# Kernel tuning notes

Hardware: AMD Instinct MI355X
Metric: run time of the kernel (lower is better)

Reference implementation:

```python
import jax, jax.numpy as jnp
import numpy as np

B, L, D_MODEL, H = 2, 2048, 2048, 16
HD = D_MODEL // H  # 128 head dim
EPS = 1e-6


def rms_norm(x, scale):
    # float32 RMSNorm over last dim, per Flux QKNorm
    x32 = x.astype(jnp.float32)
    rrms = jax.lax.rsqrt(jnp.mean(x32 * x32, axis=-1, keepdims=True) + EPS)
    return (x32 * rrms) * scale


def apply_rope(xq, xk, freqs_cis):
    # xq, xk: [B, L, H, D]; freqs_cis: [1, L, 1, D/2, 2, 2]
    shp = xq.shape
    xq_ = xq.astype(jnp.float32).reshape(*shp[:-1], -1, 1, 2)
    xk_ = xk.astype(jnp.float32).reshape(*shp[:-1], -1, 1, 2)
    xq_out = freqs_cis[..., 0] * xq_[..., 0] + freqs_cis[..., 1] * xq_[..., 1]
    xk_out = freqs_cis[..., 0] * xk_[..., 0] + freqs_cis[..., 1] * xk_[..., 1]
    return xq_out.reshape(shp).astype(xq.dtype), xk_out.reshape(shp).astype(xk.dtype)


def setup_inputs() -> dict:
    key = jax.random.key(0)
    k1, k2, k3, k4 = jax.random.split(key, 4)
    x = jax.random.normal(k1, (B, L, D_MODEL), dtype=jnp.float32)
    pe = jax.random.normal(k2, (1, L, 1, HD // 2, 2, 2), dtype=jnp.float32)
    w_qkv = jax.random.normal(k3, (D_MODEL, 3 * D_MODEL), dtype=jnp.float32) * (D_MODEL ** -0.5)
    w_proj = jax.random.normal(k4, (D_MODEL, D_MODEL), dtype=jnp.float32) * (D_MODEL ** -0.5)
    q_scale = jnp.ones((HD,), dtype=jnp.float32)
    k_scale = jnp.ones((HD,), dtype=jnp.float32)
    return {"x": x, "pe": pe, "w_qkv": w_qkv, "w_proj": w_proj,
            "q_scale": q_scale, "k_scale": k_scale}


def reference(x, pe, w_qkv, w_proj, q_scale, k_scale):
    qkv = x @ w_qkv                                  # [B, L, 3*H*D]
    qkv = qkv.reshape(B, L, 3, H, HD)
    q, k, v = qkv[:, :, 0], qkv[:, :, 1], qkv[:, :, 2]  # [B, L, H, D]
    # QK RMSNorm (cast back to v's dtype, per QKNorm.forward)
    q = rms_norm(q, q_scale).astype(v.dtype)
    k = rms_norm(k, k_scale).astype(v.dtype)
    # RoPE
    q, k = apply_rope(q, k, pe)
    # non-causal SDPA
    scale = HD ** -0.5
    scores = jnp.einsum('blhd,bmhd->bhlm', q, k) * scale
    attn = jax.nn.softmax(scores, axis=-1)
    out = jnp.einsum('bhlm,bmhd->blhd', attn, v)     # [B, L, H, D]
    out = out.reshape(B, L, H * HD)
    return out @ w_proj
```

## Files before the change

### kernel.cpp

```cpp
#include <hip/hip_runtime.h>

typedef unsigned short u16;
typedef __bf16 bf16x8 __attribute__((ext_vector_type(8)));
typedef float f32x4 __attribute__((ext_vector_type(4)));

#define DEV static __device__ __forceinline__

constexpr int Bc  = 2;
constexpr int Lc  = 2048;
constexpr int Dc  = 2048;
constexpr int Hc  = 16;
constexpr int HDc = 128;
constexpr int Mc  = Bc * Lc;
constexpr int N3c = 3 * Dc;

DEV u16 f2bf(float f) {
  unsigned u = __builtin_bit_cast(unsigned, f);
  u += 0x7fffu + ((u >> 16) & 1u);
  return (u16)(u >> 16);
}
DEV float bf2f(u16 h) { return __builtin_bit_cast(float, ((unsigned)h) << 16); }

DEV void load16(const void* g, void* l) {
  __builtin_amdgcn_global_load_lds(
      (__attribute__((address_space(1))) void*)(g),
      (__attribute__((address_space(3))) void*)(l), 16, 0, 0);
}

__global__ __launch_bounds__(256) void k_prep(const float* __restrict__ x,
                                              const float* __restrict__ w_qkv,
                                              const float* __restrict__ w_proj,
                                              u16* __restrict__ xb,
                                              u16* __restrict__ wqkvT,
                                              u16* __restrict__ wpT) {
  __shared__ u16 t[128 * 136];
  int bid = blockIdx.x;
  int tid = threadIdx.x;
  if (bid < 4096) {
    int i = bid * 256 + tid;
    const float4* s = (const float4*)x;
    float4 a = s[2 * i], b = s[2 * i + 1];
    uint4 o;
    o.x = f2bf(a.x) | ((unsigned)f2bf(a.y) << 16);
    o.y = f2bf(a.z) | ((unsigned)f2bf(a.w) << 16);
    o.z = f2bf(b.x) | ((unsigned)f2bf(b.y) << 16);
    o.w = f2bf(b.z) | ((unsigned)f2bf(b.w) << 16);
    ((uint4*)xb)[i] = o;
    return;
  }
  const float* src;
  u16* dst;
  int tiles_c;
  long ss;
  if (bid < 4096 + 768) {
    int bx = bid - 4096;
    src = w_qkv; dst = wqkvT; tiles_c = 48; ss = N3c;
    int tr = bx / tiles_c, tc = bx % tiles_c;
    src += (long)tr * 128 * ss + tc * 128;
    dst += (long)(tc * 128) * Dc + tr * 128;
  } else {
    int bx = bid - 4864;
    src = w_proj; dst = wpT; tiles_c = 16; ss = Dc;
    int tr = bx / tiles_c, tc = bx % tiles_c;
    src += (long)tr * 128 * ss + tc * 128;
    dst += (long)(tc * 128) * Dc + tr * 128;
  }
#pragma unroll
  for (int p = 0; p < 16; p++) {
    int r = p * 8 + (tid >> 5);
    int c4 = (tid & 31) * 4;
    float4 v = *(const float4*)(src + (long)r * ss + c4);
    t[(c4 + 0) * 136 + r] = f2bf(v.x);
    t[(c4 + 1) * 136 + r] = f2bf(v.y);
    t[(c4 + 2) * 136 + r] = f2bf(v.z);
    t[(c4 + 3) * 136 + r] = f2bf(v.w);
  }
  __syncthreads();
#pragma unroll
  for (int p = 0; p < 8; p++) {
    int c = p * 16 + (tid >> 4);
    int r8 = (tid & 15) * 8;
    uint4 v = *(const uint4*)&t[c * 136 + r8];
    *(uint4*)(dst + (long)c * Dc + r8) = v;
  }
}

__global__ __launch_bounds__(256) void k_vtrans(const u16* __restrict__ qkvb,
                                                u16* __restrict__ Vt) {
  int lt = blockIdx.x;
  int bh = blockIdx.y;
  int b = bh >> 4, h = bh & 15;
  const u16* s = qkvb + (long)(b * Lc + lt * 128) * N3c + 2 * Dc + h * HDc;
  u16* d = Vt + (long)bh * HDc * Lc + lt * 128;
  __shared__ u16 t[128 * 136];
  int tid = threadIdx.x;
#pragma unroll
  for (int p = 0; p < 8; p++) {
    int r = p * 16 + (tid >> 4);
    int c = (tid & 15) * 8;
    uint4 v = *(const uint4*)(s + (long)r * N3c + c);
    const u16* pv = (const u16*)&v;
#pragma unroll
    for (int j = 0; j < 8; j++) t[(c + j) * 136 + r] = pv[j];
  }
  __syncthreads();
#pragma unroll
  for (int p = 0; p < 8; p++) {
    int c = p * 16 + (tid >> 4);
    int r8 = (tid & 15) * 8;
    *(uint4*)(d + (long)c * Lc + r8) = *(const uint4*)&t[c * 136 + r8];
  }
}

DEV void cstore(float* p, float v) { *p = v; }
DEV void cstore(u16* p, float v) { *p = f2bf(v); }

template <typename OT>
__global__ __launch_bounds__(256) void k_gemm(const u16* __restrict__ A,
                                              const u16* __restrict__ Bt,
                                              OT* __restrict__ C, int M, int N,
                                              int K) {
  __shared__ u16 sA[128 * 64], sB[128 * 64];
  int nb = N >> 7;
  int brow = blockIdx.x / nb, bcol = blockIdx.x % nb;
  int tid = threadIdx.x, w = tid >> 6, lane = tid & 63;
  int wr = w >> 1, wc = w & 1, quad = lane >> 4, l15 = lane & 15;
  int lr = lane >> 3, lc = lane & 7;
  const u16* Ab = A + ((long)(brow * 128 + w * 32 + lr)) * K + (lc ^ lr) * 8;
  const u16* Bb = Bt + ((long)(bcol * 128 + w * 32 + lr)) * K + (lc ^ lr) * 8;
  u16* sAw = sA + (w * 32) * 64;
  u16* sBw = sB + (w * 32) * 64;
  f32x4 acc[4][4] = {};
  for (int k0 = 0; k0 < K; k0 += 64) {
    __syncthreads();
#pragma unroll
    for (int i = 0; i < 4; i++) {
      load16(Ab + (long)i * 8 * K + k0, sAw + i * 8 * 64);
      load16(Bb + (long)i * 8 * K + k0, sBw + i * 8 * 64);
    }
    __syncthreads();
#pragma unroll
    for (int kk = 0; kk < 2; kk++) {
      bf16x8 af[4], bfr[4];
#pragma unroll
      for (int mi = 0; mi < 4; mi++) {
        int r = wr * 64 + mi * 16 + l15;
        af[mi] = *(const bf16x8*)&sA[r * 64 + (((kk * 4 + quad) ^ (r & 7)) << 3)];
      }
#pragma unroll
      for (int ni = 0; ni < 4; ni++) {
        int r = wc * 64 + ni * 16 + l15;
        bfr[ni] = *(const bf16x8*)&sB[r * 64 + (((kk * 4 + quad) ^ (r & 7)) << 3)];
      }
#pragma unroll
      for (int mi = 0; mi < 4; mi++)
#pragma unroll
        for (int ni = 0; ni < 4; ni++)
          acc[mi][ni] =
              __builtin_amdgcn_mfma_f32_16x16x32_bf16(af[mi], bfr[ni], acc[mi][ni], 0, 0, 0);
    }
  }
  long orow = (long)brow * 128 + wr * 64;
  int ocol = bcol * 128 + wc * 64;
#pragma unroll
  for (int mi = 0; mi < 4; mi++)
#pragma unroll
    for (int ni = 0; ni < 4; ni++)
#pragma unroll
      for (int r = 0; r < 4; r++)
        cstore(&C[(orow + mi * 16 + quad * 4 + r) * (long)N + ocol + ni * 16 + l15],
               acc[mi][ni][r]);
}

__global__ __launch_bounds__(256) void k_rmsrope(const u16* __restrict__ qkvb,
                                                 const float* __restrict__ pe,
                                                 const float* __restrict__ qsc,
                                                 const float* __restrict__ ksc,
                                                 u16* __restrict__ Qr,
                                                 u16* __restrict__ Kr) {
  int row = blockIdx.x;
  int l = row & (Lc - 1);
  int b = row >> 11;
  int tid = threadIdx.x;
  int h = tid >> 4, s16 = tid & 15;
  int d0 = s16 * 8;
  const u16* qp = qkvb + (long)row * N3c + h * HDc + d0;
  uint4 qv = *(const uint4*)qp;
  uint4 kv = *(const uint4*)(qp + Dc);
  const u16* qu = (const u16*)&qv;
  const u16* ku = (const u16*)&kv;
  float q[8], k[8];
#pragma unroll
  for (int j = 0; j < 8; j++) {
    q[j] = bf2f(qu[j]);
    k[j] = bf2f(ku[j]);
  }
  float sq = 0.f, sk = 0.f;
#pragma unroll
  for (int j = 0; j < 8; j++) {
    sq += q[j] * q[j];
    sk += k[j] * k[j];
  }
#pragma unroll
  for (int m = 1; m < 16; m <<= 1) {
    sq += __shfl_xor(sq, m);
    sk += __shfl_xor(sk, m);
  }
  float rq = rsqrtf(sq * (1.f / HDc) + 1e-6f);
  float rk = rsqrtf(sk * (1.f / HDc) + 1e-6f);
  float qs8[8], ks8[8];
  *(float4*)&qs8[0] = *(const float4*)(qsc + d0);
  *(float4*)&qs8[4] = *(const float4*)(qsc + d0 + 4);
  *(float4*)&ks8[0] = *(const float4*)(ksc + d0);
  *(float4*)&ks8[4] = *(const float4*)(ksc + d0 + 4);
#pragma unroll
  for (int j = 0; j < 8; j++) {
    q[j] *= rq * qs8[j];
    k[j] *= rk * ks8[j];
  }
  float e[16];
  const float* pep = pe + (long)l * 256 + s16 * 16;
#pragma unroll
  for (int j = 0; j < 4; j++) *(float4*)&e[j * 4] = *(const float4*)(pep + j * 4);
  float qo[8], ko[8];
#pragma unroll
  for (int p = 0; p < 4; p++) {
    float e00 = e[p * 4 + 0], e01 = e[p * 4 + 1];
    float e10 = e[p * 4 + 2], e11 = e[p * 4 + 3];
    qo[2 * p]     = e00 * q[2 * p] + e01 * q[2 * p + 1];
    qo[2 * p + 1] = e10 * q[2 * p] + e11 * q[2 * p + 1];
    ko[2 * p]     = e00 * k[2 * p] + e01 * k[2 * p + 1];
    ko[2 * p + 1] = e10 * k[2 * p] + e11 * k[2 * p + 1];
  }
  constexpr float RS = 0.08838834764831845f;
  uint4 oq, ok;
  oq.x = f2bf(qo[0] * RS) | ((unsigned)f2bf(qo[1] * RS) << 16);
  oq.y = f2bf(qo[2] * RS) | ((unsigned)f2bf(qo[3] * RS) << 16);
  oq.z = f2bf(qo[4] * RS) | ((unsigned)f2bf(qo[5] * RS) << 16);
  oq.w = f2bf(qo[6] * RS) | ((unsigned)f2bf(qo[7] * RS) << 16);
  ok.x = f2bf(ko[0]) | ((unsigned)f2bf(ko[1]) << 16);
  ok.y = f2bf(ko[2]) | ((unsigned)f2bf(ko[3]) << 16);
  ok.z = f2bf(ko[4]) | ((unsigned)f2bf(ko[5]) << 16);
  ok.w = f2bf(ko[6]) | ((unsigned)f2bf(ko[7]) << 16);
  long o = (((long)(b * Hc + h)) * Lc + l) * HDc + d0;
  *(uint4*)(Qr + o) = oq;
  *(uint4*)(Kr + o) = ok;
}

__global__ __launch_bounds__(256, 3) void k_attn(const u16* __restrict__ Qr,
                                                 const u16* __restrict__ Kr,
                                                 const u16* __restrict__ Vt,
                                                 u16* __restrict__ Ao) {
  __shared__ u16 smem[24576];
  u16* sQ = smem;
  u16* sK = smem + 8192;
  u16* sV = smem + 16384;
  u16* sP = sQ;
  int bx = blockIdx.x;
  int bh = (bx & 7) | ((bx >> 8) << 3);
  int lt = (bx >> 3) & 31;
  const u16* Qg = Qr + ((long)bh * Lc + lt * 64) * HDc;
  const u16* Kg = Kr + (long)bh * Lc * HDc;
  const u16* Vg = Vt + (long)bh * HDc * Lc;
  int tid = threadIdx.x, w = tid >> 6, lane = tid & 63;
  int quad = lane >> 4, l15 = lane & 15;
  int wsl = w >> 1, wsm = w & 1;
  int wd = w >> 1, wl2 = w & 1;

#pragma unroll
  for (int i = 0; i < 4; i++) {
    int r = i * 16 + w * 4 + quad;
    int gch = l15 ^ (r & 15);
    load16(Qg + (long)r * HDc + gch * 8, sQ + (i * 16 + w * 4) * 128);
  }
  __syncthreads();
  bf16x8 qf[2][4];
#pragma unroll
  for (int mi = 0; mi < 2; mi++) {
    int l = wsl * 32 + mi * 16 + l15;
#pragma unroll
    for (int kk = 0; kk < 4; kk++)
      qf[mi][kk] = *(const bf16x8*)&sQ[l * 128 + (((kk * 4 + quad) ^ l15) << 3)];
  }

  f32x4 o[4][2] = {};
  float rs[8] = {};
  for (int t = 0; t < 32; t++) {
    int m0 = t * 64;
    __syncthreads();
#pragma unroll
    for (int i = 0; i < 4; i++) {
      int r = i * 16 + w * 4 + quad;
      int gch = l15 ^ (r & 15);
      load16(Kg + ((long)(m0 + r)) * HDc + gch * 8, sK + (i * 16 + w * 4) * 128);
    }
#pragma unroll
    for (int i = 0; i < 4; i++) {
      int r = i * 32 + w * 8 + (lane >> 3);
      int gch = (lane & 7) ^ (r & 7);
      load16(Vg + (long)r * Lc + m0 + gch * 8, sV + (i * 32 + w * 8) * 64);
    }
    __syncthreads();
    f32x4 s[2][2] = {};
#pragma unroll
    for (int kk = 0; kk < 4; kk++) {
      bf16x8 bk[2];
#pragma unroll
      for (int ni = 0; ni < 2; ni++) {
        int m = wsm * 32 + ni * 16 + l15;
        bk[ni] = *(const bf16x8*)&sK[m * 128 + (((kk * 4 + quad) ^ l15) << 3)];
      }
#pragma unroll
      for (int mi = 0; mi < 2; mi++)
#pragma unroll
        for (int ni = 0; ni < 2; ni++)
          s[mi][ni] =
              __builtin_amdgcn_mfma_f32_16x16x32_bf16(qf[mi][kk], bk[ni], s[mi][ni], 0, 0, 0);
    }
#pragma unroll
    for (int mi = 0; mi < 2; mi++)
#pragma unroll
      for (int ni = 0; ni < 2; ni++) {
        int pc = wsm * 32 + ni * 16 + l15;
#pragma unroll
        for (int r = 0; r < 4; r++) {
          int pr = wsl * 32 + mi * 16 + quad * 4 + r;
          float p = __expf(s[mi][ni][r]);
          rs[mi * 4 + r] += p;
          unsigned u = __builtin_bit_cast(unsigned, p) + 0x8000u;
          sP[pr * 64 + ((((pc >> 3) ^ (pr & 7)) << 3) | (pc & 7))] = (u16)(u >> 16);
        }
      }
    __syncthreads();
#pragma unroll
    for (int kk = 0; kk < 2; kk++) {
      bf16x8 av[4], bp[2];
#pragma unroll
      for (int mi = 0; mi < 4; mi++) {
        int d = wd * 64 + mi * 16 + l15;
        av[mi] = *(const bf16x8*)&sV[d * 64 + (((kk * 4 + quad) ^ (d & 7)) << 3)];
      }
#pragma unroll
      for (int ni = 0; ni < 2; ni++) {
        int l = wl2 * 32 + ni * 16 + l15;
        bp[ni] = *(const bf16x8*)&sP[l * 64 + (((kk * 4 + quad) ^ (l & 7)) << 3)];
      }
#pragma unroll
      for (int mi = 0; mi < 4; mi++)
#pragma unroll
        for (int ni = 0; ni < 2; ni++)
          o[mi][ni] =
              __builtin_amdgcn_mfma_f32_16x16x32_bf16(av[mi], bp[ni], o[mi][ni], 0, 0, 0);
    }
  }
  __syncthreads();
  float* red  = (float*)sK;
  float* rsum = (float*)sV;
#pragma unroll
  for (int mi = 0; mi < 2; mi++)
#pragma unroll
    for (int r = 0; r < 4; r++) {
      int l = wsl * 32 + mi * 16 + quad * 4 + r;
      red[l * 33 + wsm * 16 + l15] = rs[mi * 4 + r];
    }
  __syncthreads();
  if (tid < 64) {
    float a = 0.f;
#pragma unroll
    for (int j = 0; j < 32; j++) a += red[tid * 33 + j];
    rsum[tid] = a;
  }
  __syncthreads();
  int b = bh >> 4, h = bh & 15;
#pragma unroll
  for (int ni = 0; ni < 2; ni++) {
    int l = wl2 * 32 + ni * 16 + l15;
    float inv = 1.f / rsum[l];
    long rowb = ((long)(b * Lc + lt * 64 + l)) * Dc + h * HDc;
#pragma unroll
    for (int mi = 0; mi < 4; mi++) {
      int d = wd * 64 + mi * 16 + quad * 4;
      ushort4 pk;
      pk.x = f2bf(o[mi][ni][0] * inv);
      pk.y = f2bf(o[mi][ni][1] * inv);
      pk.z = f2bf(o[mi][ni][2] * inv);
      pk.w = f2bf(o[mi][ni][3] * inv);
      *(ushort4*)(Ao + rowb + d) = pk;
    }
  }
}

extern "C" void kernel_launch(void* const* d_in, const int* in_sizes, int n_in,
                              void* d_out, int out_size, void* d_ws, size_t ws_size,
                              hipStream_t stream) {
  const float* x      = (const float*)d_in[0];
  const float* pe     = (const float*)d_in[1];
  const float* w_qkv  = (const float*)d_in[2];
  const float* w_proj = (const float*)d_in[3];
  const float* qs     = (const float*)d_in[4];
  const float* ks     = (const float*)d_in[5];
  float* out = (float*)d_out;
  char* ws = (char*)d_ws;

  u16* xb    = (u16*)(ws);
  u16* wqkvT = (u16*)(ws + 16777216);
  u16* wpT   = (u16*)(ws + 41943040);
  u16* qkvb  = (u16*)(ws + 50331648);
  u16* Qr    = (u16*)(ws + 100663296);
  u16* Kr    = (u16*)(ws + 117440512);
  u16* Vtw   = (u16*)(ws + 134217728);
  u16* Ao    = (u16*)(ws + 150994944);

  k_prep<<<5120, 256, 0, stream>>>(x, w_qkv, w_proj, xb, wqkvT, wpT);
  k_gemm<u16><<<32 * 48, 256, 0, stream>>>(xb, wqkvT, qkvb, Mc, N3c, Dc);
  k_rmsrope<<<Mc, 256, 0, stream>>>(qkvb, pe, qs, ks, Qr, Kr);
  k_vtrans<<<dim3(16, 32), 256, 0, stream>>>(qkvb, Vtw);
  k_attn<<<32 * 32, 256, 0, stream>>>(Qr, Kr, Vtw, Ao);
  k_gemm<float><<<32 * 16, 256, 0, stream>>>(Ao, wpT, out, Mc, Dc, Dc);
}
```

Baseline: 432.3 us.

## Replace GEMM with 256-row 8-wave double-buffered pipelined kernel

Replaces the simple 128x128 single-buffered GEMM with an 8-wave, 512-thread kernel using 256xBN tiles. It double-buffers LDS, interleaves global-to-LDS prefetch with quarter-tile MFMA phases under explicit waitcnt and barriers, and raises MFMA priority with s_setprio. It also remaps block IDs in groups of eight, likely to improve L2 locality across the grid. The intent is to hide load latency and raise data reuse for both the QKV and output projections. In exchange it needs much more LDS and more registers, and the hand-written vmcnt accounting is fragile. The output GEMM also launches only 256 blocks, which may underfill the device.

Measured after the change: 434.1 us. Within noise of the previous version (+0.4%).

```diff
diff --git a/kernel.cpp b/kernel.cpp
--- a/kernel.cpp
+++ b/kernel.cpp
@@ -115,61 +115,156 @@
 DEV void cstore(float* p, float v) { *p = v; }
 DEV void cstore(u16* p, float v) { *p = f2bf(v); }
 
-template <typename OT>
-__global__ __launch_bounds__(256) void k_gemm(const u16* __restrict__ A,
-                                              const u16* __restrict__ Bt,
-                                              OT* __restrict__ C, int M, int N,
-                                              int K) {
-  __shared__ u16 sA[128 * 64], sB[128 * 64];
-  int nb = N >> 7;
-  int brow = blockIdx.x / nb, bcol = blockIdx.x % nb;
+template <int BN, typename OT>
+__global__ __launch_bounds__(512, 2) void k_gemm8(const u16* __restrict__ A,
+                                                  const u16* __restrict__ Bt,
+                                                  OT* __restrict__ C,
+                                                  int M, int N, int K) {
+  constexpr int WN = BN / 4;
+  constexpr int NF = WN / 16;
+  constexpr int BH = BN / 128;
+  __shared__ __align__(16) u16 sA[2][256 * 64];
+  __shared__ __align__(16) u16 sB[2][BN * 64];
+
+  int nb = N / BN;
+  int q8 = gridDim.x >> 3;
+  int sid = (blockIdx.x & 7) * q8 + (blockIdx.x >> 3);
+  int brow = sid / nb, bcol = sid % nb;
+
   int tid = threadIdx.x, w = tid >> 6, lane = tid & 63;
-  int wr = w >> 1, wc = w & 1, quad = lane >> 4, l15 = lane & 15;
+  int wm = w >> 2, wn = w & 3;
+  int quad = lane >> 4, l15 = lane & 15;
   int lr = lane >> 3, lc = lane & 7;
-  const u16* Ab = A + ((long)(brow * 128 + w * 32 + lr)) * K + (lc ^ lr) * 8;
-  const u16* Bb = Bt + ((long)(bcol * 128 + w * 32 + lr)) * K + (lc ^ lr) * 8;
-  u16* sAw = sA + (w * 32) * 64;
-  u16* sBw = sB + (w * 32) * 64;
-  f32x4 acc[4][4] = {};
-  for (int k0 = 0; k0 < K; k0 += 64) {
-    __syncthreads();
-#pragma unroll
-    for (int i = 0; i < 4; i++) {
-      load16(Ab + (long)i * 8 * K + k0, sAw + i * 8 * 64);
-      load16(Bb + (long)i * 8 * K + k0, sBw + i * 8 * 64);
-    }
-    __syncthreads();
-#pragma unroll
-    for (int kk = 0; kk < 2; kk++) {
-      bf16x8 af[4], bfr[4];
-#pragma unroll
-      for (int mi = 0; mi < 4; mi++) {
-        int r = wr * 64 + mi * 16 + l15;
-        af[mi] = *(const bf16x8*)&sA[r * 64 + (((kk * 4 + quad) ^ (r & 7)) << 3)];
-      }
-#pragma unroll
-      for (int ni = 0; ni < 4; ni++) {
-        int r = wc * 64 + ni * 16 + l15;
-        bfr[ni] = *(const bf16x8*)&sB[r * 64 + (((kk * 4 + quad) ^ (r & 7)) << 3)];
-      }
-#pragma unroll
-      for (int mi = 0; mi < 4; mi++)
-#pragma unroll
-        for (int ni = 0; ni < 4; ni++)
-          acc[mi][ni] =
-              __builtin_amdgcn_mfma_f32_16x16x32_bf16(af[mi], bfr[ni], acc[mi][ni], 0, 0, 0);
-    }
-  }
-  long orow = (long)brow * 128 + wr * 64;
-  int ocol = bcol * 128 + wc * 64;
-#pragma unroll
-  for (int mi = 0; mi < 4; mi++)
-#pragma unroll
-    for (int ni = 0; ni < 4; ni++)
+  int NT = K >> 6;
+
+  const u16* Ag = A + (long)(brow * 256 + w * 8 + lr) * K + (lc ^ lr) * 8;
+  const u16* Bg = Bt + (long)(bcol * BN + w * 8 + lr) * K + (lc ^ lr) * 8;
+
+  f32x4 acc[8][NF] = {};
+  bf16x8 a[4][2];
+  bf16x8 b[2][NF / 2][2];
+
+#define STAGE_A8(c, t, h)                                                      \
+  if ((t) < NT) {                                                              \
+    _Pragma("unroll") for (int j = 0; j < 2; j++)                              \
+        load16(Ag + ((long)((h)*128 + j * 64)) * K + (long)(t)*64,             \
+               &sA[c][((h)*128 + j * 64 + w * 8) * 64]);                       \
+  }
+#define STAGE_B8(c, t, h)                                                      \
+  if ((t) < NT) {                                                              \
+    _Pragma("unroll") for (int j = 0; j < BH; j++)                             \
+        load16(Bg + ((long)((h) * (BN / 2) + j * 64)) * K + (long)(t)*64,      \
+               &sB[c][((h) * (BN / 2) + j * 64 + w * 8) * 64]);                \
+  }
+#define LDA8(c, qm)                                                            \
+  _Pragma("unroll") for (int mi = 0; mi < 4; mi++) {                           \
+    int r = wm * 128 + ((qm)*4 + mi) * 16 + l15;                               \
+    _Pragma("unroll") for (int kk = 0; kk < 2; kk++)                           \
+        a[mi][kk] =                                                            \
+        *(const bf16x8*)&sA[c][r * 64 + (((kk * 4 + quad) ^ (r & 7)) << 3)];   \
+  }
+#define LDB8(c, qn)                                                            \
+  _Pragma("unroll") for (int fi = 0; fi < NF / 2; fi++) {                      \
+    int rn = wn * WN + ((qn) * (NF / 2) + fi) * 16 + l15;                      \
+    _Pragma("unroll") for (int kk = 0; kk < 2; kk++)                           \
+        b[qn][fi][kk] =                                                        \
+        *(const bf16x8*)&sB[c][rn * 64 + (((kk * 4 + quad) ^ (rn & 7)) << 3)]; \
+  }
+#define MFMAQ(qm, qn)                                                          \
+  _Pragma("unroll") for (int mi = 0; mi < 4; mi++)                             \
+  _Pragma("unroll") for (int fi = 0; fi < NF / 2; fi++)                        \
+  _Pragma("unroll") for (int kk = 0; kk < 2; kk++)                             \
+      acc[(qm)*4 + mi][(qn) * (NF / 2) + fi] =                                 \
+          __builtin_amdgcn_mfma_f32_16x16x32_bf16(                             \
+              a[mi][kk], b[qn][fi][kk],                                        \
+              acc[(qm)*4 + mi][(qn) * (NF / 2) + fi], 0, 0, 0);
+#define BAR8() __builtin_amdgcn_s_barrier()
+#define LGKM08()                                     \
+  asm volatile("s_waitcnt lgkmcnt(0)" ::: "memory"); \
+  __builtin_amdgcn_sched_barrier(0)
+#define VMC_STEADY8()                                      \
+  do {                                                     \
+    if constexpr (BH == 2)                                 \
+      asm volatile("s_waitcnt vmcnt(4)" ::: "memory");     \
+    else                                                   \
+      asm volatile("s_waitcnt vmcnt(2)" ::: "memory");     \
+  } while (0)
+
+#define TILE8(c, t)                                                            \
+  {                                                                            \
+    LDA8(c, 0);                                                                \
+    LDB8(c, 0);                                                                \
+    STAGE_A8((c) ^ 1, (t) + 1, 0);                                             \
+    BAR8();                                                                    \
+    LGKM08();                                                                  \
+    __builtin_amdgcn_s_setprio(1);                                             \
+    MFMAQ(0, 0);                                                               \
+    __builtin_amdgcn_s_setprio(0);                                             \
+    BAR8();                                                                    \
+    LDB8(c, 1);                                                                \
+    STAGE_A8((c) ^ 1, (t) + 1, 1);                                             \
+    BAR8();                                                                    \
+    LGKM08();                                                                  \
+    __builtin_amdgcn_s_setprio(1);                                             \
+    MFMAQ(0, 1);                                                               \
+    __builtin_amdgcn_s_setprio(0);                                             \
+    BAR8();                                                                    \
+    LDA8(c, 1);                                                                \
+    STAGE_B8(c, (t) + 2, 0);                                                   \
+    BAR8();                                                                    \
+    LGKM08();                                                                  \
+    __builtin_amdgcn_s_setprio(1);                                             \
+    MFMAQ(1, 1);                                                               \
+    __builtin_amdgcn_s_setprio(0);                                             \
+    BAR8();                                                                    \
+    STAGE_B8(c, (t) + 2, 1);                                                   \
+    BAR8();                                                                    \
+    __builtin_amdgcn_s_setprio(1);                                             \
+    MFMAQ(1, 0);                                                               \
+    __builtin_amdgcn_s_setprio(0);                                             \
+    if ((t) < NT - 2) {                                                        \
+      VMC_STEADY8();                                                           \
+    } else {                                                                   \
+      asm volatile("s_waitcnt vmcnt(0)" ::: "memory");                         \
+    }                                                                          \
+    __builtin_amdgcn_sched_barrier(0);                                         \
+    BAR8();                                                                    \
+  }
+
+  STAGE_A8(0, 0, 0);
+  STAGE_A8(0, 0, 1);
+  STAGE_B8(0, 0, 0);
+  STAGE_B8(0, 0, 1);
+  STAGE_B8(1, 1, 0);
+  STAGE_B8(1, 1, 1);
+  VMC_STEADY8();
+  __builtin_amdgcn_sched_barrier(0);
+  BAR8();
+
+  for (int kt = 0; kt < NT; kt += 2) {
+    TILE8(0, kt);
+    TILE8(1, kt + 1);
+  }
+
+  long orow = (long)brow * 256 + wm * 128;
+  int ocol = bcol * BN + wn * WN;
+#pragma unroll
+  for (int mi = 0; mi < 8; mi++)
+#pragma unroll
+    for (int ni = 0; ni < NF; ni++)
 #pragma unroll
       for (int r = 0; r < 4; r++)
         cstore(&C[(orow + mi * 16 + quad * 4 + r) * (long)N + ocol + ni * 16 + l15],
                acc[mi][ni][r]);
+#undef STAGE_A8
+#undef STAGE_B8
+#undef LDA8
+#undef LDB8
+#undef MFMAQ
+#undef BAR8
+#undef LGKM08
+#undef VMC_STEADY8
+#undef TILE8
 }
 
 __global__ __launch_bounds__(256) void k_rmsrope(const u16* __restrict__ qkvb,
@@ -412,9 +507,9 @@
   u16* Ao    = (u16*)(ws + 150994944);
 
   k_prep<<<5120, 256, 0, stream>>>(x, w_qkv, w_proj, xb, wqkvT, wpT);
-  k_gemm<u16><<<32 * 48, 256, 0, stream>>>(xb, wqkvT, qkvb, Mc, N3c, Dc);
+  k_gemm8<256, u16><<<16 * 24, 512, 0, stream>>>(xb, wqkvT, qkvb, Mc, N3c, Dc);
   k_rmsrope<<<Mc, 256, 0, stream>>>(qkvb, pe, qs, ks, Qr, Kr);
   k_vtrans<<<dim3(16, 32), 256, 0, stream>>>(qkvb, Vtw);
   k_attn<<<32 * 32, 256, 0, stream>>>(Qr, Kr, Vtw, Ao);
-  k_gemm<float><<<32 * 16, 256, 0, stream>>>(Ao, wpT, out, Mc, Dc, Dc);
-}
+  k_gemm8<128, float><<<16 * 16, 512, 0, stream>>>(Ao, wpT, out, Mc, Dc, Dc);
+}
```

## Replace GEMM with double-buffered 128x256 tile, 8-wave pipelined kernel

Applied to the files above, without the earlier changes.

Replaces the single-buffered 128x128 GEMM with a 512-thread kernel using 128x256 tiles, double-buffered LDS and async global-to-LDS prefetch staged across half-tiles, with manual waitcnt/barrier scheduling and setprio around MFMA bursts. It also remaps block IDs in groups of 8 for better L2 locality. The aim is to overlap global loads with MFMA compute and raise arithmetic intensity per block. In exchange it uses more LDS and yields fewer blocks (e.g. 256 for the projection GEMM, near one wave on the GPU), and the hand-tuned vmcnt counts are fragile.

New measurement: 417.0 us. 3.5% less time.

```diff
diff --git a/kernel.cpp b/kernel.cpp
--- a/kernel.cpp
+++ b/kernel.cpp
@@ -116,60 +116,125 @@
 DEV void cstore(u16* p, float v) { *p = f2bf(v); }
 
 template <typename OT>
-__global__ __launch_bounds__(256) void k_gemm(const u16* __restrict__ A,
-                                              const u16* __restrict__ Bt,
-                                              OT* __restrict__ C, int M, int N,
-                                              int K) {
-  __shared__ u16 sA[128 * 64], sB[128 * 64];
-  int nb = N >> 7;
-  int brow = blockIdx.x / nb, bcol = blockIdx.x % nb;
+__global__ __launch_bounds__(512, 2) void k_gemm2p(const u16* __restrict__ A,
+                                                   const u16* __restrict__ Bt,
+                                                   OT* __restrict__ C,
+                                                   int M, int N, int K) {
+  __shared__ __align__(16) u16 sA[2][128 * 64];
+  __shared__ __align__(16) u16 sB[2][256 * 64];
+
+  int nb = N >> 8;
+  int q8 = gridDim.x >> 3;
+  int sid = (blockIdx.x & 7) * q8 + (blockIdx.x >> 3);
+  int brow = sid / nb, bcol = sid % nb;
+
   int tid = threadIdx.x, w = tid >> 6, lane = tid & 63;
-  int wr = w >> 1, wc = w & 1, quad = lane >> 4, l15 = lane & 15;
+  int wm = w >> 2, wn = w & 3;
+  int quad = lane >> 4, l15 = lane & 15;
   int lr = lane >> 3, lc = lane & 7;
-  const u16* Ab = A + ((long)(brow * 128 + w * 32 + lr)) * K + (lc ^ lr) * 8;
-  const u16* Bb = Bt + ((long)(bcol * 128 + w * 32 + lr)) * K + (lc ^ lr) * 8;
-  u16* sAw = sA + (w * 32) * 64;
-  u16* sBw = sB + (w * 32) * 64;
+  int NT = K >> 6;
+
+  const u16* Ag = A + (long)(brow * 128 + w * 8 + lr) * K + (lc ^ lr) * 8;
+  const u16* Bg = Bt + (long)(bcol * 256 + w * 8 + lr) * K + (lc ^ lr) * 8;
+
   f32x4 acc[4][4] = {};
-  for (int k0 = 0; k0 < K; k0 += 64) {
-    __syncthreads();
-#pragma unroll
-    for (int i = 0; i < 4; i++) {
-      load16(Ab + (long)i * 8 * K + k0, sAw + i * 8 * 64);
-      load16(Bb + (long)i * 8 * K + k0, sBw + i * 8 * 64);
-    }
-    __syncthreads();
-#pragma unroll
-    for (int kk = 0; kk < 2; kk++) {
-      bf16x8 af[4], bfr[4];
-#pragma unroll
-      for (int mi = 0; mi < 4; mi++) {
-        int r = wr * 64 + mi * 16 + l15;
-        af[mi] = *(const bf16x8*)&sA[r * 64 + (((kk * 4 + quad) ^ (r & 7)) << 3)];
-      }
-#pragma unroll
-      for (int ni = 0; ni < 4; ni++) {
-        int r = wc * 64 + ni * 16 + l15;
-        bfr[ni] = *(const bf16x8*)&sB[r * 64 + (((kk * 4 + quad) ^ (r & 7)) << 3)];
-      }
-#pragma unroll
-      for (int mi = 0; mi < 4; mi++)
-#pragma unroll
-        for (int ni = 0; ni < 4; ni++)
-          acc[mi][ni] =
-              __builtin_amdgcn_mfma_f32_16x16x32_bf16(af[mi], bfr[ni], acc[mi][ni], 0, 0, 0);
-    }
-  }
-  long orow = (long)brow * 128 + wr * 64;
-  int ocol = bcol * 128 + wc * 64;
+  bf16x8 a[2][2];
+  bf16x8 b[4][2];
+
+#define STAGE_A(c, t)                                                          \
+  if ((t) < NT) {                                                              \
+    _Pragma("unroll") for (int j = 0; j < 2; j++)                              \
+        load16(Ag + (long)(j * 64) * K + (long)(t) * 64,                       \
+               &sA[c][(j * 64 + w * 8) * 64]);                                 \
+  }
+#define STAGE_B(c, t)                                                          \
+  if ((t) < NT) {                                                              \
+    _Pragma("unroll") for (int j = 0; j < 4; j++)                              \
+        load16(Bg + (long)(j * 64) * K + (long)(t) * 64,                       \
+               &sB[c][(j * 64 + w * 8) * 64]);                                 \
+  }
+#define LDA(c, qm)                                                             \
+  _Pragma("unroll") for (int mi = 0; mi < 2; mi++) {                           \
+    int r = wm * 64 + ((qm)*2 + mi) * 16 + l15;                                \
+    _Pragma("unroll") for (int kk = 0; kk < 2; kk++)                           \
+        a[mi][kk] =                                                            \
+        *(const bf16x8*)&sA[c][r * 64 + (((kk * 4 + quad) ^ (r & 7)) << 3)];   \
+  }
+#define LDB(c)                                                                 \
+  _Pragma("unroll") for (int fi = 0; fi < 4; fi++) {                           \
+    int rn = wn * 64 + fi * 16 + l15;                                          \
+    _Pragma("unroll") for (int kk = 0; kk < 2; kk++)                           \
+        b[fi][kk] =                                                            \
+        *(const bf16x8*)&sB[c][rn * 64 + (((kk * 4 + quad) ^ (rn & 7)) << 3)]; \
+  }
+#define MFMAH(qm)                                                              \
+  _Pragma("unroll") for (int mi = 0; mi < 2; mi++)                             \
+  _Pragma("unroll") for (int fi = 0; fi < 4; fi++)                             \
+  _Pragma("unroll") for (int kk = 0; kk < 2; kk++)                             \
+      acc[(qm)*2 + mi][fi] = __builtin_amdgcn_mfma_f32_16x16x32_bf16(          \
+          a[mi][kk], b[fi][kk], acc[(qm)*2 + mi][fi], 0, 0, 0);
+#define BAR() __builtin_amdgcn_s_barrier()
+#define LGKM0()                                      \
+  asm volatile("s_waitcnt lgkmcnt(0)" ::: "memory"); \
+  __builtin_amdgcn_sched_barrier(0)
+
+#define TILE(c, t)                                                             \
+  {                                                                            \
+    LDA(c, 0);                                                                 \
+    LDB(c);                                                                    \
+    STAGE_A((c) ^ 1, (t) + 1);                                                 \
+    BAR();                                                                     \
+    LGKM0();                                                                   \
+    __builtin_amdgcn_s_setprio(1);                                             \
+    MFMAH(0);                                                                  \
+    __builtin_amdgcn_s_setprio(0);                                             \
+    BAR();                                                                     \
+    LDA(c, 1);                                                                 \
+    STAGE_B(c, (t) + 2);                                                       \
+    BAR();                                                                     \
+    LGKM0();                                                                   \
+    __builtin_amdgcn_s_setprio(1);                                             \
+    MFMAH(1);                                                                  \
+    __builtin_amdgcn_s_setprio(0);                                             \
+    if ((t) < NT - 2) {                                                        \
+      asm volatile("s_waitcnt vmcnt(4)" ::: "memory");                         \
+    } else {                                                                   \
+      asm volatile("s_waitcnt vmcnt(0)" ::: "memory");                         \
+    }                                                                          \
+    __builtin_amdgcn_sched_barrier(0);                                         \
+    BAR();                                                                     \
+  }
+
+  STAGE_A(0, 0);
+  STAGE_B(0, 0);
+  STAGE_B(1, 1);
+  asm volatile("s_waitcnt vmcnt(4)" ::: "memory");
+  __builtin_amdgcn_sched_barrier(0);
+  BAR();
+
+  for (int kt = 0; kt < NT; kt += 2) {
+    TILE(0, kt);
+    TILE(1, kt + 1);
+  }
+
+  long orow = (long)brow * 128 + wm * 64;
+  int ocol = bcol * 256 + wn * 64;
 #pragma unroll
   for (int mi = 0; mi < 4; mi++)
 #pragma unroll
-    for (int ni = 0; ni < 4; ni++)
+    for (int fi = 0; fi < 4; fi++)
 #pragma unroll
       for (int r = 0; r < 4; r++)
-        cstore(&C[(orow + mi * 16 + quad * 4 + r) * (long)N + ocol + ni * 16 + l15],
-               acc[mi][ni][r]);
+        cstore(&C[(orow + mi * 16 + quad * 4 + r) * (long)N + ocol + fi * 16 + l15],
+               acc[mi][fi][r]);
+#undef STAGE_A
+#undef STAGE_B
+#undef LDA
+#undef LDB
+#undef MFMAH
+#undef BAR
+#undef LGKM0
+#undef TILE
 }
 
 __global__ __launch_bounds__(256) void k_rmsrope(const u16* __restrict__ qkvb,
@@ -412,9 +477,9 @@
   u16* Ao    = (u16*)(ws + 150994944);
 
   k_prep<<<5120, 256, 0, stream>>>(x, w_qkv, w_proj, xb, wqkvT, wpT);
-  k_gemm<u16><<<32 * 48, 256, 0, stream>>>(xb, wqkvT, qkvb, Mc, N3c, Dc);
+  k_gemm2p<u16><<<32 * 24, 512, 0, stream>>>(xb, wqkvT, qkvb, Mc, N3c, Dc);
   k_rmsrope<<<Mc, 256, 0, stream>>>(qkvb, pe, qs, ks, Qr, Kr);
   k_vtrans<<<dim3(16, 32), 256, 0, stream>>>(qkvb, Vtw);
   k_attn<<<32 * 32, 256, 0, stream>>>(Qr, Kr, Vtw, Ao);
-  k_gemm<float><<<32 * 16, 256, 0, stream>>>(Ao, wpT, out, Mc, Dc, Dc);
-}
+  k_gemm2p<float><<<32 * 8, 512, 0, stream>>>(Ao, wpT, out, Mc, Dc, Dc);
+}
```
